# Kernel tuning notes

Hardware: AMD Instinct MI355X
Metric: run time of the kernel (lower is better)

## Reference

```python
import jax, jax.numpy as jnp
import numpy as np

N = 100000
E = 1600000
D_IN = 128
D_H = 128
D_OUT = 64
BN_EPS = 1e-5


def setup_inputs() -> dict:
    key = jax.random.key(0)
    ks = jax.random.split(key, 32)
    inp = {}
    inp["x"] = jax.random.normal(ks[0], (N, D_IN), dtype=jnp.float32)
    inp["edge_index"] = jax.random.randint(ks[1], (2, E), 0, N, dtype=jnp.int32)
    def lin(k, fan_in, fan_out):
        b = 1.0 / np.sqrt(fan_in)
        return jax.random.uniform(k, (fan_in, fan_out), jnp.float32, -b, b)
    # conv0: MLP [128,128,128]
    inp["W1_0"] = lin(ks[2], D_IN, D_H); inp["b1_0"] = jnp.zeros((D_H,), jnp.float32)
    inp["W2_0"] = lin(ks[3], D_H, D_H);  inp["b2_0"] = jnp.zeros((D_H,), jnp.float32)
    # conv1: MLP [128,128,128]
    inp["W1_1"] = lin(ks[4], D_H, D_H);  inp["b1_1"] = jnp.zeros((D_H,), jnp.float32)
    inp["W2_1"] = lin(ks[5], D_H, D_H);  inp["b2_1"] = jnp.zeros((D_H,), jnp.float32)
    # conv2 (last): MLP [128,128,64]
    inp["W1_2"] = lin(ks[6], D_H, D_H);  inp["b1_2"] = jnp.zeros((D_H,), jnp.float32)
    inp["W2_2"] = lin(ks[7], D_H, D_OUT); inp["b2_2"] = jnp.zeros((D_OUT,), jnp.float32)
    # BatchNorm (eval-mode) params for the 2 hidden layers
    for i, kk in zip((0, 1), (ks[8], ks[9])):
        inp[f"g{i}"] = jnp.ones((D_H,), jnp.float32)
        inp[f"be{i}"] = jnp.zeros((D_H,), jnp.float32)
        inp[f"m{i}"] = jax.random.normal(kk, (D_H,), jnp.float32) * 0.1
        inp[f"v{i}"] = jnp.ones((D_H,), jnp.float32)
    return inp


def _gin_conv(x, src, dst, W1, b1, W2, b2):
    # sum aggregation over incoming edges: out_i = x_i + sum_{j->i} x_j  (eps=0)
    agg = x + jax.ops.segment_sum(x[src], dst, num_segments=N)
    h = jax.nn.relu(agg @ W1 + b1)  # MLP hidden (dropout inactive in eval)
    return h @ W2 + b2


def _bn(h, g, be, m, v):
    return (h - m) * jax.lax.rsqrt(v + BN_EPS) * g + be


def reference(x, edge_index, W1_0, b1_0, W2_0, b2_0, W1_1, b1_1, W2_1, b2_1,
              W1_2, b1_2, W2_2, b2_2, g0, be0, m0, v0, g1, be1, m1, v1):
    src, dst = edge_index[0], edge_index[1]
    # layer 0
    out = _gin_conv(x, src, dst, W1_0, b1_0, W2_0, b2_0)
    out = _bn(out, g0, be0, m0, v0)
    x = jax.nn.relu(out) + x  # downsample is identity (in==hidden)
    # layer 1
    out = _gin_conv(x, src, dst, W1_1, b1_1, W2_1, b2_1)
    out = _bn(out, g1, be1, m1, v1)
    x = jax.nn.relu(out) + x
    # last conv + log_softmax
    out = _gin_conv(x, src, dst, W1_2, b1_2, W2_2, b2_2)
    return jax.nn.log_softmax(out, axis=-1)
```

## Files before the change

### kernel.cpp

```cpp
#include <hip/hip_runtime.h>
#include <math.h>

#define NN 100000
#define NE 1600000
#define BN_EPS 1e-5f
#define NB 782
#define BCAP 4096
#define EPB 4096
#define NEB ((NE + EPB - 1) / EPB)

typedef short bf16x8 __attribute__((ext_vector_type(8)));
typedef float f32x4 __attribute__((ext_vector_type(4)));
typedef float f32x2 __attribute__((ext_vector_type(2)));
typedef unsigned short ushort;
typedef ushort us8 __attribute__((ext_vector_type(8)));
typedef ushort us4 __attribute__((ext_vector_type(4)));
typedef unsigned ui2 __attribute__((ext_vector_type(2)));

__device__ __forceinline__ ushort f2bf(float f) {
    unsigned u = __float_as_uint(f);
    unsigned r = (u + 0x7FFFu + ((u >> 16) & 1u)) >> 16;
    return (ushort)r;
}
__device__ __forceinline__ float bf2f(ushort h) { return __uint_as_float(((unsigned)h) << 16); }

__device__ __forceinline__ void fp8x8_f32(ui2 q, float* f) {
    f32x2 p;
    p = __builtin_amdgcn_cvt_pk_f32_fp8((int)q[0], false); f[0] = p[0]; f[1] = p[1];
    p = __builtin_amdgcn_cvt_pk_f32_fp8((int)q[0], true);  f[2] = p[0]; f[3] = p[1];
    p = __builtin_amdgcn_cvt_pk_f32_fp8((int)q[1], false); f[4] = p[0]; f[5] = p[1];
    p = __builtin_amdgcn_cvt_pk_f32_fp8((int)q[1], true);  f[6] = p[0]; f[7] = p[1];
}
__device__ __forceinline__ ui2 f32_fp8x8(const float* f) {
    int d0 = __builtin_amdgcn_cvt_pk_fp8_f32(f[0], f[1], 0, false);
    d0 = __builtin_amdgcn_cvt_pk_fp8_f32(f[2], f[3], d0, true);
    int d1 = __builtin_amdgcn_cvt_pk_fp8_f32(f[4], f[5], 0, false);
    d1 = __builtin_amdgcn_cvt_pk_fp8_f32(f[6], f[7], d1, true);
    ui2 r; r[0] = (unsigned)d0; r[1] = (unsigned)d1; return r;
}

__global__ __launch_bounds__(1024) void binit_k(int* __restrict__ bcur) {
    int t = threadIdx.x;
    if (t < NB) bcur[t] = t << 12;
}

__global__ __launch_bounds__(256) void bscat_k(const int* __restrict__ ei, int* __restrict__ bcur,
                                               unsigned* __restrict__ packed) {
    __shared__ int h[NB];
    for (int i = threadIdx.x; i < NB; i += 256) h[i] = 0;
    __syncthreads();
    int base = blockIdx.x * EPB;
    for (int i = threadIdx.x; i < EPB; i += 256) {
        int e = base + i;
        if (e < NE) atomicAdd(&h[ei[NE + e] >> 7], 1);
    }
    __syncthreads();
    for (int i = threadIdx.x; i < NB; i += 256) {
        int c = h[i];
        if (c) h[i] = atomicAdd(&bcur[i], c);
    }
    __syncthreads();
    for (int i = threadIdx.x; i < EPB; i += 256) {
        int e = base + i;
        if (e < NE) {
            int d = ei[NE + e];
            int b = d >> 7;
            int pos = atomicAdd(&h[b], 1);
            packed[pos] = (unsigned)ei[e] | ((unsigned)(d & 127) << 17);
        }
    }
}

__global__ __launch_bounds__(256) void csr_k(unsigned* __restrict__ packed,
                                             const int* __restrict__ bcur,
                                             int* __restrict__ rpS, int* __restrict__ rpE) {
    __shared__ unsigned ent[BCAP];
    __shared__ int hc[128], hb[128], sc[128];
    int t = threadIdx.x, b = blockIdx.x;
    int base = b << 12;
    int nb = bcur[b] - base;
    if (nb > BCAP) nb = BCAP;
    for (int i = t; i < nb; i += 256) ent[i] = packed[base + i];
    if (t < 128) hc[t] = 0;
    __syncthreads();
    for (int i = t; i < nb; i += 256) atomicAdd(&hc[ent[i] >> 17], 1);
    __syncthreads();
    if (t < 128) sc[t] = hc[t];
    __syncthreads();
    for (int off = 1; off < 128; off <<= 1) {
        int u = 0;
        if (t < 128 && t >= off) u = sc[t - off];
        __syncthreads();
        if (t < 128) sc[t] += u;
        __syncthreads();
    }
    if (t < 128) {
        int ex = sc[t] - hc[t];
        hb[t] = ex;
        int node = b * 128 + t;
        if (node < NN) {
            rpS[node] = base + ex;
            rpE[node] = base + sc[t];
        }
    }
    __syncthreads();
    for (int i = t; i < nb; i += 256) {
        unsigned u = ent[i];
        int pos = atomicAdd(&hb[u >> 17], 1);
        packed[base + pos] = u & 0x1FFFFu;
    }
}

__global__ __launch_bounds__(256) void cvtx_k(const float* __restrict__ x, ushort* __restrict__ xb,
                                              unsigned* __restrict__ xq) {
    int i = blockIdx.x * 256 + threadIdx.x;
    float4 v = ((const float4*)x)[i];
    us4 o;
    o[0] = f2bf(v.x); o[1] = f2bf(v.y); o[2] = f2bf(v.z); o[3] = f2bf(v.w);
    ((us4*)xb)[i] = o;
    int d = __builtin_amdgcn_cvt_pk_fp8_f32(v.x, v.y, 0, false);
    d = __builtin_amdgcn_cvt_pk_fp8_f32(v.z, v.w, d, true);
    xq[i] = (unsigned)d;
}

__global__ __launch_bounds__(256) void packall_k(
    const float* __restrict__ Wa, const float* __restrict__ Wb, const float* __restrict__ Wc,
    const float* __restrict__ Wd, const float* __restrict__ We, const float* __restrict__ Wf_,
    ushort* __restrict__ Fa, ushort* __restrict__ Fb, ushort* __restrict__ Fc,
    ushort* __restrict__ Fd, ushort* __restrict__ Fe, ushort* __restrict__ Ff) {
    int which = blockIdx.x >> 3, sub = blockIdx.x & 7;
    const float* W; ushort* F; int DOUT = 128;
    switch (which) {
        case 0: W = Wa; F = Fa; break;
        case 1: W = Wb; F = Fb; break;
        case 2: W = Wc; F = Fc; break;
        case 3: W = Wd; F = Fd; break;
        case 4: W = We; F = Fe; break;
        default: W = Wf_; F = Ff; DOUT = 64; break;
    }
    int NT = DOUT / 16;
    int idx = sub * 256 + threadIdx.x;
    if (idx >= 4 * NT * 64) return;
    int l = idx & 63;
    int nt = (idx >> 6) % NT;
    int kt = idx / (NT * 64);
    int colw = nt * 16 + (l & 15);
    int k0 = kt * 32 + (l >> 4) * 8;
    us8 o;
#pragma unroll
    for (int e = 0; e < 8; ++e) o[e] = f2bf(W[(k0 + e) * DOUT + colw]);
    ((us8*)F)[idx] = o;
}

template <int FINAL>
__global__ __launch_bounds__(256, 4) void fused_k(
    const ushort* __restrict__ X, const unsigned* __restrict__ XQ,
    const int* __restrict__ rpS, const int* __restrict__ rpE,
    const unsigned* __restrict__ col,
    const ushort* __restrict__ W1f, const ushort* __restrict__ W2f,
    const float* __restrict__ b1, const float* __restrict__ b2,
    const float* __restrict__ bng, const float* __restrict__ bnb,
    const float* __restrict__ bnm, const float* __restrict__ bnv,
    ushort* __restrict__ outb, unsigned* __restrict__ outq, float* __restrict__ outf) {
    __shared__ ushort Alds[8192];
    __shared__ ushort Hlds[8192];
    const int t = threadIdx.x;
    const int w = t >> 6, l = t & 63;
    const int lrow = l & 15, lchk = l >> 4;
    const int R0 = blockIdx.x * 64;
    const us8* __restrict__ xv = (const us8*)X;
    const ui2* __restrict__ xq2 = (const ui2*)XQ;

    const int ch = t & 15;
#pragma unroll
    for (int it = 0; it < 4; ++it) {
        int nl = it * 16 + (t >> 4);
        int node = R0 + nl;
        float a[8];
#pragma unroll
        for (int i = 0; i < 8; ++i) a[i] = 0.f;
        if (node < NN) {
            us8 self = xv[(size_t)node * 16 + ch];
#pragma unroll
            for (int i = 0; i < 8; ++i) a[i] = bf2f(self[i]);
            int p = rpS[node];
            const int pe = rpE[node];
            for (; p + 7 < pe; p += 8) {
                unsigned s[8];
#pragma unroll
                for (int u = 0; u < 8; ++u) s[u] = col[p + u];
                ui2 v[8];
#pragma unroll
                for (int u = 0; u < 8; ++u) v[u] = xq2[(size_t)s[u] * 16 + ch];
#pragma unroll
                for (int u = 0; u < 8; ++u) {
                    float f[8];
                    fp8x8_f32(v[u], f);
#pragma unroll
                    for (int i = 0; i < 8; ++i) a[i] += f[i];
                }
            }
            for (; p + 3 < pe; p += 4) {
                ui2 v0 = xq2[(size_t)col[p] * 16 + ch];
                ui2 v1 = xq2[(size_t)col[p + 1] * 16 + ch];
                ui2 v2 = xq2[(size_t)col[p + 2] * 16 + ch];
                ui2 v3 = xq2[(size_t)col[p + 3] * 16 + ch];
                float f0[8], f1[8], f2[8], f3[8];
                fp8x8_f32(v0, f0); fp8x8_f32(v1, f1); fp8x8_f32(v2, f2); fp8x8_f32(v3, f3);
#pragma unroll
                for (int i = 0; i < 8; ++i) a[i] += (f0[i] + f1[i]) + (f2[i] + f3[i]);
            }
            for (; p < pe; ++p) {
                ui2 v = xq2[(size_t)col[p] * 16 + ch];
                float f[8];
                fp8x8_f32(v, f);
#pragma unroll
                for (int i = 0; i < 8; ++i) a[i] += f[i];
            }
        }
        us8 o;
#pragma unroll
        for (int i = 0; i < 8; ++i) o[i] = f2bf(a[i]);
        int byte = (nl * 256 + ch * 16) ^ ((nl & 7) << 4);
        *(us8*)((char*)Alds + byte) = o;
    }

    const bf16x8* __restrict__ w1p = (const bf16x8*)W1f;
    bf16x8 w1r[2][4];
#pragma unroll
    for (int ntl = 0; ntl < 2; ++ntl)
#pragma unroll
        for (int kt = 0; kt < 4; ++kt)
            w1r[ntl][kt] = w1p[(kt * 8 + (2 * w + ntl)) * 64 + l];

    __syncthreads();

#pragma unroll
    for (int mt = 0; mt < 4; ++mt) {
        bf16x8 af[4];
#pragma unroll
        for (int kt = 0; kt < 4; ++kt) {
            int row = mt * 16 + lrow;
            int byte = (row * 256 + kt * 64 + lchk * 16) ^ ((row & 7) << 4);
            af[kt] = *(const bf16x8*)((char*)Alds + byte);
        }
        f32x4 acc[2] = {f32x4{0.f, 0.f, 0.f, 0.f}, f32x4{0.f, 0.f, 0.f, 0.f}};
#pragma unroll
        for (int kt = 0; kt < 4; ++kt)
#pragma unroll
            for (int ntl = 0; ntl < 2; ++ntl)
                acc[ntl] = __builtin_amdgcn_mfma_f32_16x16x32_bf16(af[kt], w1r[ntl][kt], acc[ntl], 0, 0, 0);
#pragma unroll
        for (int ntl = 0; ntl < 2; ++ntl) {
            int colb = (2 * w + ntl) * 16 + lrow;
            float bias = b1[colb];
#pragma unroll
            for (int r = 0; r < 4; ++r) {
                int rloc = mt * 16 + lchk * 4 + r;
                float hv = fmaxf(acc[ntl][r] + bias, 0.f);
                int byte = (rloc * 256 + colb * 2) ^ ((rloc & 7) << 4);
                *(ushort*)((char*)Hlds + byte) = f2bf(hv);
            }
        }
    }
    __syncthreads();

    if constexpr (FINAL == 0) {
        const bf16x8* __restrict__ w2p = (const bf16x8*)W2f;
        bf16x8 w2r[2][4];
#pragma unroll
        for (int ntl = 0; ntl < 2; ++ntl)
#pragma unroll
            for (int kt = 0; kt < 4; ++kt)
                w2r[ntl][kt] = w2p[(kt * 8 + (2 * w + ntl)) * 64 + l];
        float sc[2], of[2];
#pragma unroll
        for (int ntl = 0; ntl < 2; ++ntl) {
            int colb = (2 * w + ntl) * 16 + lrow;
            sc[ntl] = bng[colb] * rsqrtf(bnv[colb] + BN_EPS);
            of[ntl] = (b2[colb] - bnm[colb]) * sc[ntl] + bnb[colb];
        }
#pragma unroll
        for (int mt = 0; mt < 4; ++mt) {
            bf16x8 hf[4];
#pragma unroll
            for (int kt = 0; kt < 4; ++kt) {
                int row = mt * 16 + lrow;
                int byte = (row * 256 + kt * 64 + lchk * 16) ^ ((row & 7) << 4);
                hf[kt] = *(const bf16x8*)((char*)Hlds + byte);
            }
            f32x4 acc2[2] = {f32x4{0.f, 0.f, 0.f, 0.f}, f32x4{0.f, 0.f, 0.f, 0.f}};
#pragma unroll
            for (int kt = 0; kt < 4; ++kt)
#pragma unroll
                for (int ntl = 0; ntl < 2; ++ntl)
                    acc2[ntl] = __builtin_amdgcn_mfma_f32_16x16x32_bf16(hf[kt], w2r[ntl][kt], acc2[ntl], 0, 0, 0);
#pragma unroll
            for (int ntl = 0; ntl < 2; ++ntl) {
                int colb = (2 * w + ntl) * 16 + lrow;
#pragma unroll
                for (int r = 0; r < 4; ++r) {
                    int rloc = mt * 16 + lchk * 4 + r;
                    float o = fmaxf(acc2[ntl][r] * sc[ntl] + of[ntl], 0.f);
                    int byte = (rloc * 256 + colb * 2) ^ ((rloc & 7) << 4);
                    *(ushort*)((char*)Alds + byte) = f2bf(o);
                }
            }
        }
        __syncthreads();
        us8* __restrict__ ob8 = (us8*)outb;
        ui2* __restrict__ oq2 = (ui2*)outq;
#pragma unroll
        for (int j = 0; j < 4; ++j) {
            int i = t + 256 * j;
            int row = i >> 4, chunk = i & 15;
            int grow = R0 + row;
            if (grow < NN) {
                int byte = (row * 256 + chunk * 16) ^ ((row & 7) << 4);
                us8 h8 = *(const us8*)((char*)Alds + byte);
                us8 r8 = xv[(size_t)grow * 16 + chunk];
                float oo[8];
#pragma unroll
                for (int e = 0; e < 8; ++e) oo[e] = bf2f(h8[e]) + bf2f(r8[e]);
                us8 o8;
#pragma unroll
                for (int e = 0; e < 8; ++e) o8[e] = f2bf(oo[e]);
                ob8[(size_t)grow * 16 + chunk] = o8;
                oq2[(size_t)grow * 16 + chunk] = f32_fp8x8(oo);
            }
        }
    } else {
        const bf16x8* __restrict__ w2p = (const bf16x8*)W2f;
        bf16x8 hf[4];
#pragma unroll
        for (int kt = 0; kt < 4; ++kt) {
            int row = w * 16 + lrow;
            int byte = (row * 256 + kt * 64 + lchk * 16) ^ ((row & 7) << 4);
            hf[kt] = *(const bf16x8*)((char*)Hlds + byte);
        }
        f32x4 acc2[4];
#pragma unroll
        for (int nt = 0; nt < 4; ++nt) acc2[nt] = f32x4{0.f, 0.f, 0.f, 0.f};
#pragma unroll
        for (int kt = 0; kt < 4; ++kt)
#pragma unroll
            for (int nt = 0; nt < 4; ++nt)
                acc2[nt] = __builtin_amdgcn_mfma_f32_16x16x32_bf16(hf[kt], w2p[(kt * 4 + nt) * 64 + l], acc2[nt], 0, 0, 0);
        float bb[4];
#pragma unroll
        for (int nt = 0; nt < 4; ++nt) bb[nt] = b2[nt * 16 + lrow];
#pragma unroll
        for (int r = 0; r < 4; ++r) {
            float v0 = acc2[0][r] + bb[0], v1 = acc2[1][r] + bb[1];
            float v2 = acc2[2][r] + bb[2], v3 = acc2[3][r] + bb[3];
            float mx = fmaxf(fmaxf(v0, v1), fmaxf(v2, v3));
            for (int d = 1; d < 16; d <<= 1) mx = fmaxf(mx, __shfl_xor(mx, d));
            float sm = expf(v0 - mx) + expf(v1 - mx) + expf(v2 - mx) + expf(v3 - mx);
            for (int d = 1; d < 16; d <<= 1) sm += __shfl_xor(sm, d);
            float L = mx + logf(sm);
            int grow = R0 + w * 16 + lchk * 4 + r;
            if (grow < NN) {
                outf[(size_t)grow * 64 + 0 + lrow] = v0 - L;
                outf[(size_t)grow * 64 + 16 + lrow] = v1 - L;
                outf[(size_t)grow * 64 + 32 + lrow] = v2 - L;
                outf[(size_t)grow * 64 + 48 + lrow] = v3 - L;
            }
        }
    }
}

extern "C" void kernel_launch(void* const* d_in, const int* in_sizes, int n_in,
                              void* d_out, int out_size, void* d_ws, size_t ws_size,
                              hipStream_t stream) {
    const float* x = (const float*)d_in[0];
    const int* ei = (const int*)d_in[1];
    const float* W1_0 = (const float*)d_in[2];
    const float* b1_0 = (const float*)d_in[3];
    const float* W2_0 = (const float*)d_in[4];
    const float* b2_0 = (const float*)d_in[5];
    const float* W1_1 = (const float*)d_in[6];
    const float* b1_1 = (const float*)d_in[7];
    const float* W2_1 = (const float*)d_in[8];
    const float* b2_1 = (const float*)d_in[9];
    const float* W1_2 = (const float*)d_in[10];
    const float* b1_2 = (const float*)d_in[11];
    const float* W2_2 = (const float*)d_in[12];
    const float* b2_2 = (const float*)d_in[13];
    const float* g0 = (const float*)d_in[14];
    const float* be0 = (const float*)d_in[15];
    const float* m0 = (const float*)d_in[16];
    const float* v0 = (const float*)d_in[17];
    const float* g1 = (const float*)d_in[18];
    const float* be1 = (const float*)d_in[19];
    const float* m1 = (const float*)d_in[20];
    const float* v1 = (const float*)d_in[21];
    float* out = (float*)d_out;

    char* ws = (char*)d_ws;
    ushort* xb0 = (ushort*)(ws);
    ushort* xb1 = (ushort*)(ws + 25600000);
    unsigned* xq0 = (unsigned*)(ws + 51200000);
    unsigned* xq1 = (unsigned*)(ws + 64000000);
    unsigned* packed = (unsigned*)(ws + 76800000);
    int* rpS = (int*)(ws + 76800000 + 12812288);
    int* rpE = (int*)(ws + 76800000 + 12812288 + 400128);
    int* bcur = (int*)(ws + 76800000 + 12812288 + 800256);
    ushort* W10f = (ushort*)(ws + 76800000 + 12812288 + 800256 + 4096);
    ushort* W20f = W10f + 16384;
    ushort* W11f = W20f + 16384;
    ushort* W21f = W11f + 16384;
    ushort* W12f = W21f + 16384;
    ushort* W22f = W12f + 16384;

    binit_k<<<1, 1024, 0, stream>>>(bcur);
    bscat_k<<<NEB, 256, 0, stream>>>(ei, bcur, packed);
    csr_k<<<NB, 256, 0, stream>>>(packed, bcur, rpS, rpE);

    cvtx_k<<<12500, 256, 0, stream>>>(x, xb0, xq0);
    packall_k<<<48, 256, 0, stream>>>(W1_0, W2_0, W1_1, W2_1, W1_2, W2_2,
                                      W10f, W20f, W11f, W21f, W12f, W22f);

    const int GG = (NN + 63) / 64;

    fused_k<0><<<GG, 256, 0, stream>>>(xb0, xq0, rpS, rpE, packed, W10f, W20f, b1_0, b2_0,
                                       g0, be0, m0, v0, xb1, xq1, nullptr);
    fused_k<0><<<GG, 256, 0, stream>>>(xb1, xq1, rpS, rpE, packed, W11f, W21f, b1_1, b2_1,
                                       g1, be1, m1, v1, xb0, xq0, nullptr);
    fused_k<1><<<GG, 256, 0, stream>>>(xb0, xq0, rpS, rpE, packed, W12f, W22f, b1_2, b2_2,
                                       nullptr, nullptr, nullptr, nullptr, nullptr, nullptr, out);
}
```

Measured before the change: 245.8 us.

## Shrink fused GIN tile to 32 rows, gather 16-byte fp8 chunks per lane

The fused aggregation+MLP kernel now processes 32 nodes per block instead of 64, halving LDS use and raising the launch-bounds occupancy hint from 4 to 6 blocks per CU. In the gather, each thread handles one node with 8 lanes per row loading 16-byte fp8 chunks (16 features) instead of 8-byte chunks, giving fewer, wider loads and more nodes in flight. Bounds checks are dropped because 100000 divides evenly by 32, and in the final layer only two waves do the second GEMM. The trade-off is more registers per thread for 16 accumulators, longer per-thread edge loops with less unrolling, and twice as many blocks.

```diff
diff --git a/kernel.cpp b/kernel.cpp
--- a/kernel.cpp
+++ b/kernel.cpp
@@ -16,6 +16,7 @@
 typedef ushort us8 __attribute__((ext_vector_type(8)));
 typedef ushort us4 __attribute__((ext_vector_type(4)));
 typedef unsigned ui2 __attribute__((ext_vector_type(2)));
+typedef unsigned ui4 __attribute__((ext_vector_type(4)));
 
 __device__ __forceinline__ ushort f2bf(float f) {
     unsigned u = __float_as_uint(f);
@@ -24,12 +25,16 @@
 }
 __device__ __forceinline__ float bf2f(ushort h) { return __uint_as_float(((unsigned)h) << 16); }
 
-__device__ __forceinline__ void fp8x8_f32(ui2 q, float* f) {
+__device__ __forceinline__ void fp8x16_f32(ui4 q, float* f) {
     f32x2 p;
-    p = __builtin_amdgcn_cvt_pk_f32_fp8((int)q[0], false); f[0] = p[0]; f[1] = p[1];
-    p = __builtin_amdgcn_cvt_pk_f32_fp8((int)q[0], true);  f[2] = p[0]; f[3] = p[1];
-    p = __builtin_amdgcn_cvt_pk_f32_fp8((int)q[1], false); f[4] = p[0]; f[5] = p[1];
-    p = __builtin_amdgcn_cvt_pk_f32_fp8((int)q[1], true);  f[6] = p[0]; f[7] = p[1];
+    p = __builtin_amdgcn_cvt_pk_f32_fp8((int)q[0], false); f[0] = p[0];  f[1] = p[1];
+    p = __builtin_amdgcn_cvt_pk_f32_fp8((int)q[0], true);  f[2] = p[0];  f[3] = p[1];
+    p = __builtin_amdgcn_cvt_pk_f32_fp8((int)q[1], false); f[4] = p[0];  f[5] = p[1];
+    p = __builtin_amdgcn_cvt_pk_f32_fp8((int)q[1], true);  f[6] = p[0];  f[7] = p[1];
+    p = __builtin_amdgcn_cvt_pk_f32_fp8((int)q[2], false); f[8] = p[0];  f[9] = p[1];
+    p = __builtin_amdgcn_cvt_pk_f32_fp8((int)q[2], true);  f[10] = p[0]; f[11] = p[1];
+    p = __builtin_amdgcn_cvt_pk_f32_fp8((int)q[3], false); f[12] = p[0]; f[13] = p[1];
+    p = __builtin_amdgcn_cvt_pk_f32_fp8((int)q[3], true);  f[14] = p[0]; f[15] = p[1];
 }
 __device__ __forceinline__ ui2 f32_fp8x8(const float* f) {
     int d0 = __builtin_amdgcn_cvt_pk_fp8_f32(f[0], f[1], 0, false);
@@ -153,7 +158,7 @@
 }
 
 template <int FINAL>
-__global__ __launch_bounds__(256, 4) void fused_k(
+__global__ __launch_bounds__(256, 6) void fused_k(
     const ushort* __restrict__ X, const unsigned* __restrict__ XQ,
     const int* __restrict__ rpS, const int* __restrict__ rpE,
     const unsigned* __restrict__ col,
@@ -162,67 +167,51 @@
     const float* __restrict__ bng, const float* __restrict__ bnb,
     const float* __restrict__ bnm, const float* __restrict__ bnv,
     ushort* __restrict__ outb, unsigned* __restrict__ outq, float* __restrict__ outf) {
-    __shared__ ushort Alds[8192];
-    __shared__ ushort Hlds[8192];
+    __shared__ ushort Alds[4096];
+    __shared__ ushort Hlds[4096];
     const int t = threadIdx.x;
     const int w = t >> 6, l = t & 63;
     const int lrow = l & 15, lchk = l >> 4;
-    const int R0 = blockIdx.x * 64;
+    const int R0 = blockIdx.x * 32;
     const us8* __restrict__ xv = (const us8*)X;
-    const ui2* __restrict__ xq2 = (const ui2*)XQ;
-
-    const int ch = t & 15;
-#pragma unroll
-    for (int it = 0; it < 4; ++it) {
-        int nl = it * 16 + (t >> 4);
-        int node = R0 + nl;
-        float a[8];
-#pragma unroll
-        for (int i = 0; i < 8; ++i) a[i] = 0.f;
-        if (node < NN) {
-            us8 self = xv[(size_t)node * 16 + ch];
-#pragma unroll
-            for (int i = 0; i < 8; ++i) a[i] = bf2f(self[i]);
-            int p = rpS[node];
-            const int pe = rpE[node];
-            for (; p + 7 < pe; p += 8) {
-                unsigned s[8];
-#pragma unroll
-                for (int u = 0; u < 8; ++u) s[u] = col[p + u];
-                ui2 v[8];
-#pragma unroll
-                for (int u = 0; u < 8; ++u) v[u] = xq2[(size_t)s[u] * 16 + ch];
-#pragma unroll
-                for (int u = 0; u < 8; ++u) {
-                    float f[8];
-                    fp8x8_f32(v[u], f);
-#pragma unroll
-                    for (int i = 0; i < 8; ++i) a[i] += f[i];
-                }
-            }
-            for (; p + 3 < pe; p += 4) {
-                ui2 v0 = xq2[(size_t)col[p] * 16 + ch];
-                ui2 v1 = xq2[(size_t)col[p + 1] * 16 + ch];
-                ui2 v2 = xq2[(size_t)col[p + 2] * 16 + ch];
-                ui2 v3 = xq2[(size_t)col[p + 3] * 16 + ch];
-                float f0[8], f1[8], f2[8], f3[8];
-                fp8x8_f32(v0, f0); fp8x8_f32(v1, f1); fp8x8_f32(v2, f2); fp8x8_f32(v3, f3);
-#pragma unroll
-                for (int i = 0; i < 8; ++i) a[i] += (f0[i] + f1[i]) + (f2[i] + f3[i]);
-            }
-            for (; p < pe; ++p) {
-                ui2 v = xq2[(size_t)col[p] * 16 + ch];
-                float f[8];
-                fp8x8_f32(v, f);
-#pragma unroll
-                for (int i = 0; i < 8; ++i) a[i] += f[i];
-            }
-        }
-        us8 o;
-#pragma unroll
-        for (int i = 0; i < 8; ++i) o[i] = f2bf(a[i]);
-        int byte = (nl * 256 + ch * 16) ^ ((nl & 7) << 4);
-        *(us8*)((char*)Alds + byte) = o;
+    const ui4* __restrict__ xq4 = (const ui4*)XQ;
+
+    {
+        const int ch = t & 7;
+        const int nl = t >> 3;
+        const int node = R0 + nl;
+        float a[16];
+        us8 s0 = xv[(size_t)node * 16 + 2 * ch];
+        us8 s1 = xv[(size_t)node * 16 + 2 * ch + 1];
+#pragma unroll
+        for (int i = 0; i < 8; ++i) { a[i] = bf2f(s0[i]); a[8 + i] = bf2f(s1[i]); }
+        int p = rpS[node];
+        const int pe = rpE[node];
+        for (; p + 3 < pe; p += 4) {
+            unsigned c0 = col[p], c1 = col[p + 1], c2 = col[p + 2], c3 = col[p + 3];
+            ui4 v0 = xq4[(size_t)c0 * 8 + ch];
+            ui4 v1 = xq4[(size_t)c1 * 8 + ch];
+            ui4 v2 = xq4[(size_t)c2 * 8 + ch];
+            ui4 v3 = xq4[(size_t)c3 * 8 + ch];
+            float f0[16], f1[16], f2[16], f3[16];
+            fp8x16_f32(v0, f0); fp8x16_f32(v1, f1); fp8x16_f32(v2, f2); fp8x16_f32(v3, f3);
+#pragma unroll
+            for (int i = 0; i < 16; ++i) a[i] += (f0[i] + f1[i]) + (f2[i] + f3[i]);
+        }
+        for (; p < pe; ++p) {
+            ui4 v = xq4[(size_t)col[p] * 8 + ch];
+            float f[16];
+            fp8x16_f32(v, f);
+#pragma unroll
+            for (int i = 0; i < 16; ++i) a[i] += f[i];
+        }
+        us8 o0, o1;
+#pragma unroll
+        for (int i = 0; i < 8; ++i) { o0[i] = f2bf(a[i]); o1[i] = f2bf(a[8 + i]); }
+        int byte0 = (nl * 256 + (2 * ch) * 16) ^ ((nl & 7) << 4);
+        int byte1 = (nl * 256 + (2 * ch + 1) * 16) ^ ((nl & 7) << 4);
+        *(us8*)((char*)Alds + byte0) = o0;
+        *(us8*)((char*)Alds + byte1) = o1;
     }
 
     const bf16x8* __restrict__ w1p = (const bf16x8*)W1f;
@@ -236,7 +225,7 @@
     __syncthreads();
 
 #pragma unroll
-    for (int mt = 0; mt < 4; ++mt) {
+    for (int mt = 0; mt < 2; ++mt) {
         bf16x8 af[4];
 #pragma unroll
         for (int kt = 0; kt < 4; ++kt) {
@@ -281,7 +270,7 @@
             of[ntl] = (b2[colb] - bnm[colb]) * sc[ntl] + bnb[colb];
         }
 #pragma unroll
-        for (int mt = 0; mt < 4; ++mt) {
+        for (int mt = 0; mt < 2; ++mt) {
             bf16x8 hf[4];
 #pragma unroll
             for (int kt = 0; kt < 4; ++kt) {
@@ -311,55 +300,53 @@
         us8* __restrict__ ob8 = (us8*)outb;
         ui2* __restrict__ oq2 = (ui2*)outq;
 #pragma unroll
-        for (int j = 0; j < 4; ++j) {
+        for (int j = 0; j < 2; ++j) {
             int i = t + 256 * j;
             int row = i >> 4, chunk = i & 15;
             int grow = R0 + row;
-            if (grow < NN) {
-                int byte = (row * 256 + chunk * 16) ^ ((row & 7) << 4);
-                us8 h8 = *(const us8*)((char*)Alds + byte);
-                us8 r8 = xv[(size_t)grow * 16 + chunk];
-                float oo[8];
-#pragma unroll
-                for (int e = 0; e < 8; ++e) oo[e] = bf2f(h8[e]) + bf2f(r8[e]);
-                us8 o8;
-#pragma unroll
-                for (int e = 0; e < 8; ++e) o8[e] = f2bf(oo[e]);
-                ob8[(size_t)grow * 16 + chunk] = o8;
-                oq2[(size_t)grow * 16 + chunk] = f32_fp8x8(oo);
+            int byte = (row * 256 + chunk * 16) ^ ((row & 7) << 4);
+            us8 h8 = *(const us8*)((char*)Alds + byte);
+            us8 r8 = xv[(size_t)grow * 16 + chunk];
+            float oo[8];
+#pragma unroll
+            for (int e = 0; e < 8; ++e) oo[e] = bf2f(h8[e]) + bf2f(r8[e]);
+            us8 o8;
+#pragma unroll
+            for (int e = 0; e < 8; ++e) o8[e] = f2bf(oo[e]);
+            ob8[(size_t)grow * 16 + chunk] = o8;
+            oq2[(size_t)grow * 16 + chunk] = f32_fp8x8(oo);
+        }
+    } else {
+        if (w < 2) {
+            const bf16x8* __restrict__ w2p = (const bf16x8*)W2f;
+            bf16x8 hf[4];
+#pragma unroll
+            for (int kt = 0; kt < 4; ++kt) {
+                int row = w * 16 + lrow;
+                int byte = (row * 256 + kt * 64 + lchk * 16) ^ ((row & 7) << 4);
+                hf[kt] = *(const bf16x8*)((char*)Hlds + byte);
             }
-        }
-    } else {
-        const bf16x8* __restrict__ w2p = (const bf16x8*)W2f;
-        bf16x8 hf[4];
-#pragma unroll
-        for (int kt = 0; kt < 4; ++kt) {
-            int row = w * 16 + lrow;
-            int byte = (row * 256 + kt * 64 + lchk * 16) ^ ((row & 7) << 4);
-            hf[kt] = *(const bf16x8*)((char*)Hlds + byte);
-        }
-        f32x4 acc2[4];
-#pragma unroll
-        for (int nt = 0; nt < 4; ++nt) acc2[nt] = f32x4{0.f, 0.f, 0.f, 0.f};
-#pragma unroll
-        for (int kt = 0; kt < 4; ++kt)
-#pragma unroll
-            for (int nt = 0; nt < 4; ++nt)
-                acc2[nt] = __builtin_amdgcn_mfma_f32_16x16x32_bf16(hf[kt], w2p[(kt * 4 + nt) * 64 + l], acc2[nt], 0, 0, 0);
-        float bb[4];
-#pragma unroll
-        for (int nt = 0; nt < 4; ++nt) bb[nt] = b2[nt * 16 + lrow];
-#pragma unroll
-        for (int r = 0; r < 4; ++r) {
-            float v0 = acc2[0][r] + bb[0], v1 = acc2[1][r] + bb[1];
-            float v2 = acc2[2][r] + bb[2], v3 = acc2[3][r] + bb[3];
-            float mx = fmaxf(fmaxf(v0, v1), fmaxf(v2, v3));
-            for (int d = 1; d < 16; d <<= 1) mx = fmaxf(mx, __shfl_xor(mx, d));
-            float sm = expf(v0 - mx) + expf(v1 - mx) + expf(v2 - mx) + expf(v3 - mx);
-            for (int d = 1; d < 16; d <<= 1) sm += __shfl_xor(sm, d);
-            float L = mx + logf(sm);
-            int grow = R0 + w * 16 + lchk * 4 + r;
-            if (grow < NN) {
+            f32x4 acc2[4];
+#pragma unroll
+            for (int nt = 0; nt < 4; ++nt) acc2[nt] = f32x4{0.f, 0.f, 0.f, 0.f};
+#pragma unroll
+            for (int kt = 0; kt < 4; ++kt)
+#pragma unroll
+                for (int nt = 0; nt < 4; ++nt)
+                    acc2[nt] = __builtin_amdgcn_mfma_f32_16x16x32_bf16(hf[kt], w2p[(kt * 4 + nt) * 64 + l], acc2[nt], 0, 0, 0);
+            float bb[4];
+#pragma unroll
+            for (int nt = 0; nt < 4; ++nt) bb[nt] = b2[nt * 16 + lrow];
+#pragma unroll
+            for (int r = 0; r < 4; ++r) {
+                float v0 = acc2[0][r] + bb[0], v1 = acc2[1][r] + bb[1];
+                float v2 = acc2[2][r] + bb[2], v3 = acc2[3][r] + bb[3];
+                float mx = fmaxf(fmaxf(v0, v1), fmaxf(v2, v3));
+                for (int d = 1; d < 16; d <<= 1) mx = fmaxf(mx, __shfl_xor(mx, d));
+                float sm = expf(v0 - mx) + expf(v1 - mx) + expf(v2 - mx) + expf(v3 - mx);
+                for (int d = 1; d < 16; d <<= 1) sm += __shfl_xor(sm, d);
+                float L = mx + logf(sm);
+                int grow = R0 + w * 16 + lchk * 4 + r;
                 outf[(size_t)grow * 64 + 0 + lrow] = v0 - L;
                 outf[(size_t)grow * 64 + 16 + lrow] = v1 - L;
                 outf[(size_t)grow * 64 + 32 + lrow] = v2 - L;
@@ -420,7 +407,7 @@
     packall_k<<<48, 256, 0, stream>>>(W1_0, W2_0, W1_1, W2_1, W1_2, W2_2,
                                       W10f, W20f, W11f, W21f, W12f, W22f);
 
-    const int GG = (NN + 63) / 64;
+    const int GG = NN / 32;
 
     fused_k<0><<<GG, 256, 0, stream>>>(xb0, xq0, rpS, rpE, packed, W10f, W20f, b1_0, b2_0,
                                        g0, be0, m0, v0, xb1, xq1, nullptr);
```

Result: slower. 260.0 us (+5.8%).
